# Kernel tuning notes

Measured on AMD Instinct MI355X. Metric: run time of the kernel, lower is better.

## Reference

```python
import jax, jax.numpy as jnp
import numpy as np

B, T, C, H = 2, 2048, 1024, 16
HS = C // H  # 64
EPS = 1e-5


def layernorm(x, g, b):
    mu = jnp.mean(x, axis=-1, keepdims=True)
    var = jnp.var(x, axis=-1, keepdims=True)
    return (x - mu) * jax.lax.rsqrt(var + EPS) * g + b


def setup_inputs() -> dict:
    key = jax.random.key(0)
    ks = jax.random.split(key, 12)
    s = lambda fan_in: 1.0 / np.sqrt(fan_in)
    inp = {
        'x':  jax.random.normal(ks[0], (B, T, C), dtype=jnp.float32),
        'Wq': jax.random.uniform(ks[1], (H, C, HS), jnp.float32, -s(C), s(C)),
        'Wk': jax.random.uniform(ks[2], (H, C, HS), jnp.float32, -s(C), s(C)),
        'Wv': jax.random.uniform(ks[3], (H, C, HS), jnp.float32, -s(C), s(C)),
        'Wp': jax.random.uniform(ks[4], (C, C), jnp.float32, -s(C), s(C)),
        'bp': jax.random.uniform(ks[5], (C,), jnp.float32, -s(C), s(C)),
        'W1': jax.random.uniform(ks[6], (C, 4 * C), jnp.float32, -s(C), s(C)),
        'b1': jax.random.uniform(ks[7], (4 * C,), jnp.float32, -s(C), s(C)),
        'W2': jax.random.uniform(ks[8], (4 * C, C), jnp.float32, -s(4 * C), s(4 * C)),
        'b2': jax.random.uniform(ks[9], (C,), jnp.float32, -s(4 * C), s(4 * C)),
        'g1': jnp.ones((C,), jnp.float32),
        'be1': jnp.zeros((C,), jnp.float32),
        'g2': jnp.ones((C,), jnp.float32),
        'be2': jnp.zeros((C,), jnp.float32),
    }
    return inp


def block(x, Wq, Wk, Wv, Wp, bp, W1, b1, W2, b2, g1, be1, g2, be2):
    # quirky residual structure: residual is taken from the post-LN tensor
    x = layernorm(x, g1, be1)
    # batched multi-head attention (all heads at once): [B,H,T,HS]
    q = jnp.einsum('btc,hcd->bhtd', x, Wq)
    k = jnp.einsum('btc,hcd->bhtd', x, Wk)
    v = jnp.einsum('btc,hcd->bhtd', x, Wv)
    # NOTE: original scales by full embedding dim C ** -0.5, not head_size
    scores = jnp.einsum('bhtd,bhsd->bhts', q, k) * (C ** -0.5)
    causal = jnp.tril(jnp.ones((T, T), dtype=bool))
    scores = jnp.where(causal, scores, -jnp.inf)
    wei = jax.nn.softmax(scores, axis=-1)  # dropout p=0 in eval
    out = jnp.einsum('bhts,bhsd->bhtd', wei, v)
    out = out.transpose(0, 2, 1, 3).reshape(B, T, C)  # concat heads
    out = out @ Wp + bp
    x = x + out
    x = layernorm(x, g2, be2)
    ff = jax.nn.relu(x @ W1 + b1) @ W2 + b2
    return x + ff


def reference(x, Wq, Wk, Wv, Wp, bp, W1, b1, W2, b2, g1, be1, g2, be2):
    return block(x, Wq, Wk, Wv, Wp, bp, W1, b1, W2, b2, g1, be1, g2, be2)
```

## Files before the change

kernel.cpp:

```cpp
#include <hip/hip_runtime.h>
#include <hip/hip_bf16.h>
#include <cstdint>
#include <cstddef>

typedef __attribute__((ext_vector_type(8))) short short8;
typedef __attribute__((ext_vector_type(4))) float f32x4;
typedef __attribute__((ext_vector_type(16))) float f32x16;
typedef unsigned int u32;
typedef unsigned short u16;

__device__ inline u16 f2b(float x) {
    union { float f; u32 u; } v; v.f = x;
    u32 u = v.u;
    u32 r = (u + 0x7fff + ((u >> 16) & 1)) >> 16;
    return (u16)r;
}
__device__ inline float b2f(u16 h) {
    union { u32 u; float f; } v; v.u = ((u32)h) << 16;
    return v.f;
}
__device__ inline u32 cvtpk(float lo, float hi) {
    u32 r; asm("v_cvt_pk_bf16_f32 %0, %1, %2" : "=v"(r) : "v"(lo), "v"(hi)); return r;
}
__device__ inline float ex2(float x) {
    float r; asm("v_exp_f32 %0, %1" : "=v"(r) : "v"(x)); return r;
}
__device__ inline void gll16(const void* g, void* l) {
    __builtin_amdgcn_global_load_lds(
        (const __attribute__((address_space(1))) void*)g,
        (__attribute__((address_space(3))) void*)l, 16, 0, 0);
}

__global__ __launch_bounds__(256) void repack_qkv_tiled(
    const float* __restrict__ Wq, const float* __restrict__ Wk, const float* __restrict__ Wv,
    u16* __restrict__ out)
{
    __shared__ u16 lds[64 * 72];
    const int tid = threadIdx.x;
    const int c0 = blockIdx.x * 64;
    const int sh = blockIdx.y;
    const int sel = sh >> 4, h = sh & 15;
    const float* W = (sel == 0) ? Wq : (sel == 1) ? Wk : Wv;
    #pragma unroll
    for (int it = 0; it < 4; ++it) {
        int idx = tid + it * 256;
        int c = idx >> 4, d4 = idx & 15;
        float4 v = *reinterpret_cast<const float4*>(&W[((size_t)(h * 1024 + c0 + c)) * 64 + d4 * 4]);
        lds[(d4 * 4 + 0) * 72 + c] = f2b(v.x);
        lds[(d4 * 4 + 1) * 72 + c] = f2b(v.y);
        lds[(d4 * 4 + 2) * 72 + c] = f2b(v.z);
        lds[(d4 * 4 + 3) * 72 + c] = f2b(v.w);
    }
    __syncthreads();
    #pragma unroll
    for (int it = 0; it < 2; ++it) {
        int idx = tid + it * 256;
        int d = idx >> 3, c8 = idx & 7;
        short8 s = *reinterpret_cast<const short8*>(&lds[d * 72 + c8 * 8]);
        *reinterpret_cast<short8*>(&out[((size_t)(sel * 1024 + h * 64 + d)) * 1024 + c0 + c8 * 8]) = s;
    }
}

__global__ __launch_bounds__(256) void trans_tiled(
    const float* __restrict__ in, u16* __restrict__ out, int P, int Q)
{
    __shared__ u16 lds[64 * 72];
    const int tid = threadIdx.x;
    const int p0 = blockIdx.x * 64, q0 = blockIdx.y * 64;
    #pragma unroll
    for (int it = 0; it < 4; ++it) {
        int idx = tid + it * 256;
        int p = idx >> 4, q4 = idx & 15;
        float4 v = *reinterpret_cast<const float4*>(&in[(size_t)(p0 + p) * Q + q0 + q4 * 4]);
        lds[(q4 * 4 + 0) * 72 + p] = f2b(v.x);
        lds[(q4 * 4 + 1) * 72 + p] = f2b(v.y);
        lds[(q4 * 4 + 2) * 72 + p] = f2b(v.z);
        lds[(q4 * 4 + 3) * 72 + p] = f2b(v.w);
    }
    __syncthreads();
    #pragma unroll
    for (int it = 0; it < 2; ++it) {
        int idx = tid + it * 256;
        int q = idx >> 3, p8 = idx & 7;
        short8 s = *reinterpret_cast<const short8*>(&lds[q * 72 + p8 * 8]);
        *reinterpret_cast<short8*>(&out[(size_t)(q0 + q) * P + p0 + p8 * 8]) = s;
    }
}

__global__ __launch_bounds__(256) void vt_kernel(
    const u16* __restrict__ qkv, u16* __restrict__ vt)
{
    __shared__ u16 lds[64 * 72];
    const int tid = threadIdx.x;
    const int s0 = blockIdx.x * 64, h = blockIdx.y, b = blockIdx.z;
    #pragma unroll
    for (int it = 0; it < 2; ++it) {
        int idx = tid + it * 256;
        int s = idx >> 3, d8 = idx & 7;
        short8 kv = *reinterpret_cast<const short8*>(
            &qkv[((size_t)(b * 2048 + s0 + s)) * 3072 + 2048 + h * 64 + d8 * 8]);
        #pragma unroll
        for (int j = 0; j < 8; ++j) lds[(d8 * 8 + j) * 72 + s] = (u16)kv[j];
    }
    __syncthreads();
    #pragma unroll
    for (int it = 0; it < 2; ++it) {
        int idx = tid + it * 256;
        int d = idx >> 3, s8 = idx & 7;
        short8 s = *reinterpret_cast<const short8*>(&lds[d * 72 + s8 * 8]);
        *reinterpret_cast<short8*>(&vt[((size_t)(b * 16 + h) * 64 + d) * 2048 + s0 + s8 * 8]) = s;
    }
}

__global__ __launch_bounds__(256) void ln_kernel(
    const float* __restrict__ x, const float* __restrict__ g, const float* __restrict__ be,
    float* __restrict__ yf, u16* __restrict__ yb)
{
    int row = blockIdx.x;
    const float4 v = reinterpret_cast<const float4*>(x + (size_t)row * 1024)[threadIdx.x];
    float s  = v.x + v.y + v.z + v.w;
    float s2 = v.x * v.x + v.y * v.y + v.z * v.z + v.w * v.w;
    #pragma unroll
    for (int o = 32; o >= 1; o >>= 1) { s += __shfl_xor(s, o); s2 += __shfl_xor(s2, o); }
    __shared__ float red[8];
    int w = threadIdx.x >> 6;
    if ((threadIdx.x & 63) == 0) { red[w] = s; red[4 + w] = s2; }
    __syncthreads();
    s  = red[0] + red[1] + red[2] + red[3];
    s2 = red[4] + red[5] + red[6] + red[7];
    float mu = s * (1.0f / 1024.0f);
    float var = s2 * (1.0f / 1024.0f) - mu * mu;
    float rs = rsqrtf(var + 1e-5f);
    const float4 gg = reinterpret_cast<const float4*>(g)[threadIdx.x];
    const float4 bb = reinterpret_cast<const float4*>(be)[threadIdx.x];
    float4 o;
    o.x = (v.x - mu) * rs * gg.x + bb.x;
    o.y = (v.y - mu) * rs * gg.y + bb.y;
    o.z = (v.z - mu) * rs * gg.z + bb.z;
    o.w = (v.w - mu) * rs * gg.w + bb.w;
    reinterpret_cast<float4*>(yf + (size_t)row * 1024)[threadIdx.x] = o;
    uint2 pk;
    pk.x = (u32)f2b(o.x) | ((u32)f2b(o.y) << 16);
    pk.y = (u32)f2b(o.z) | ((u32)f2b(o.w) << 16);
    reinterpret_cast<uint2*>(yb + (size_t)row * 1024)[threadIdx.x] = pk;
}

template<bool BIAS, bool RELU, bool RESID, bool OUTB>
__global__ __launch_bounds__(256) void gemm_bt(
    const u16* __restrict__ A, int lda,
    const u16* __restrict__ BT, int ldb,
    void* __restrict__ out, int ldo,
    const float* __restrict__ bias,
    const float* __restrict__ resid,
    int K)
{
    __shared__ __align__(16) char smem[64 * 1024];
    const int tid = threadIdx.x;
    const int lane = tid & 63, w = tid >> 6;
    const int wr = w >> 1, wc = w & 1;
    const int l15 = lane & 15, lq = lane >> 4;

    const int nx = gridDim.x;
    const int nwg = nx * gridDim.y;
    int orig = blockIdx.y * nx + blockIdx.x;
    int wgid = orig;
    if ((nwg & 7) == 0) wgid = (orig & 7) * (nwg >> 3) + (orig >> 3);
    const int m0 = (wgid / nx) * 128, n0 = (wgid % nx) * 128;

    auto stage = [&](int kt, int buf) {
        char* As = smem + buf * 32768;
        char* Bs = smem + buf * 32768 + 16384;
        #pragma unroll
        for (int it = 0; it < 4; ++it) {
            int slot = it * 256 + tid;
            int row = slot >> 3, c8 = (slot & 7) ^ (row & 7);
            gll16(A + (size_t)(m0 + row) * lda + kt + c8 * 8, As + (it * 256 + w * 64) * 16);
        }
        #pragma unroll
        for (int it = 0; it < 4; ++it) {
            int slot = it * 256 + tid;
            int row = slot >> 3, c8 = (slot & 7) ^ (row & 7);
            gll16(BT + (size_t)(n0 + row) * ldb + kt + c8 * 8, Bs + (it * 256 + w * 64) * 16);
        }
    };

    f32x4 acc[4][4] = {};
    const int nk = K >> 6;

    stage(0, 0);
    asm volatile("s_waitcnt vmcnt(0)" ::: "memory");
    __builtin_amdgcn_s_barrier();

    for (int t = 0; t < nk; ++t) {
        const char* As = smem + (t & 1) * 32768;
        const char* Bs = smem + (t & 1) * 32768 + 16384;
        if (t + 1 < nk) {
            stage((t + 1) << 6, (t + 1) & 1);
            asm volatile("s_waitcnt vmcnt(8)" ::: "memory");
        } else {
            asm volatile("s_waitcnt vmcnt(0)" ::: "memory");
        }
        __builtin_amdgcn_s_barrier();

        #pragma unroll
        for (int kk = 0; kk < 2; ++kk) {
            const int sc = kk * 4 + lq;
            short8 a[4], b[4];
            #pragma unroll
            for (int mi = 0; mi < 4; ++mi) {
                int row = wr * 64 + mi * 16 + l15;
                a[mi] = *reinterpret_cast<const short8*>(As + row * 128 + ((sc ^ (row & 7)) << 4));
            }
            #pragma unroll
            for (int ni = 0; ni < 4; ++ni) {
                int row = wc * 64 + ni * 16 + l15;
                b[ni] = *reinterpret_cast<const short8*>(Bs + row * 128 + ((sc ^ (row & 7)) << 4));
            }
            #pragma unroll
            for (int mi = 0; mi < 4; ++mi)
                #pragma unroll
                for (int ni = 0; ni < 4; ++ni)
                    acc[mi][ni] = __builtin_amdgcn_mfma_f32_16x16x32_bf16(a[mi], b[ni], acc[mi][ni], 0, 0, 0);
        }

        asm volatile("" ::: "memory");
        __builtin_amdgcn_s_barrier();
    }

    #pragma unroll
    for (int mi = 0; mi < 4; ++mi) {
        #pragma unroll
        for (int ni = 0; ni < 4; ++ni) {
            int col = n0 + wc * 64 + ni * 16 + l15;
            float bv = BIAS ? bias[col] : 0.0f;
            #pragma unroll
            for (int r = 0; r < 4; ++r) {
                int row = m0 + wr * 64 + mi * 16 + lq * 4 + r;
                float v = acc[mi][ni][r] + bv;
                if (RELU) v = v > 0.0f ? v : 0.0f;
                if (RESID) v += resid[(size_t)row * ldo + col];
                if (OUTB) ((u16*)out)[(size_t)row * ldo + col] = f2b(v);
                else      ((float*)out)[(size_t)row * ldo + col] = v;
            }
        }
    }
}

template<bool BIAS, bool RELU, bool OUTB>
__global__ __launch_bounds__(512) void gemm_bt256(
    const u16* __restrict__ A, int lda,
    const u16* __restrict__ BT, int ldb,
    void* __restrict__ out, int ldo,
    const float* __restrict__ bias,
    int K)
{
    __shared__ __align__(16) char smem[128 * 1024];
    const int tid = threadIdx.x;
    const int lane = tid & 63, wid = tid >> 6;
    const int wm = wid >> 2, wn = wid & 3;
    const int l15 = lane & 15, lq = lane >> 4;

    const int nx = gridDim.x;
    const int nwg = nx * gridDim.y;
    int orig = blockIdx.y * nx + blockIdx.x;
    int wgid = orig;
    if ((nwg & 7) == 0) wgid = (orig & 7) * (nwg >> 3) + (orig >> 3);
    const int m0 = (wgid / nx) * 256, n0 = (wgid % nx) * 256;

    auto stage = [&](int kt, int buf) {
        char* As = smem + buf * 65536;
        char* Bs = smem + buf * 65536 + 32768;
        #pragma unroll
        for (int i = 0; i < 4; ++i) {
            int slot = i * 512 + tid;
            int row = slot >> 3, c8 = (slot & 7) ^ (row & 7);
            gll16(A + (size_t)(m0 + row) * lda + kt + c8 * 8, As + (i * 512 + wid * 64) * 16);
        }
        #pragma unroll
        for (int i = 0; i < 4; ++i) {
            int slot = i * 512 + tid;
            int row = slot >> 3, c8 = (slot & 7) ^ (row & 7);
            gll16(BT + (size_t)(n0 + row) * ldb + kt + c8 * 8, Bs + (i * 512 + wid * 64) * 16);
        }
    };

    f32x4 acc[8][4] = {};
    const int nk = K >> 6;

    stage(0, 0);
    asm volatile("s_waitcnt vmcnt(0)" ::: "memory");
    __builtin_amdgcn_s_barrier();

    for (int t = 0; t < nk; ++t) {
        const char* As = smem + (t & 1) * 65536;
        const char* Bs = smem + (t & 1) * 65536 + 32768;
        if (t + 1 < nk) {
            stage((t + 1) << 6, (t + 1) & 1);
            asm volatile("s_waitcnt vmcnt(8)" ::: "memory");
        } else {
            asm volatile("s_waitcnt vmcnt(0)" ::: "memory");
        }
        __builtin_amdgcn_s_barrier();

        #pragma unroll
        for (int kk = 0; kk < 2; ++kk) {
            const int sc = kk * 4 + lq;
            short8 a[8], b[4];
            #pragma unroll
            for (int mi = 0; mi < 8; ++mi) {
                int row = wm * 128 + mi * 16 + l15;
                a[mi] = *reinterpret_cast<const short8*>(As + row * 128 + ((sc ^ (row & 7)) << 4));
            }
            #pragma unroll
            for (int ni = 0; ni < 4; ++ni) {
                int row = wn * 64 + ni * 16 + l15;
                b[ni] = *reinterpret_cast<const short8*>(Bs + row * 128 + ((sc ^ (row & 7)) << 4));
            }
            #pragma unroll
            for (int mi = 0; mi < 8; ++mi)
                #pragma unroll
                for (int ni = 0; ni < 4; ++ni)
                    acc[mi][ni] = __builtin_amdgcn_mfma_f32_16x16x32_bf16(a[mi], b[ni], acc[mi][ni], 0, 0, 0);
        }

        asm volatile("" ::: "memory");
        __builtin_amdgcn_s_barrier();
    }

    #pragma unroll
    for (int mi = 0; mi < 8; ++mi) {
        #pragma unroll
        for (int ni = 0; ni < 4; ++ni) {
            int col = n0 + wn * 64 + ni * 16 + l15;
            float bv = BIAS ? bias[col] : 0.0f;
            #pragma unroll
            for (int r = 0; r < 4; ++r) {
                int row = m0 + wm * 128 + mi * 16 + lq * 4 + r;
                float v = acc[mi][ni][r] + bv;
                if (RELU) v = v > 0.0f ? v : 0.0f;
                if (OUTB) ((u16*)out)[(size_t)row * ldo + col] = f2b(v);
                else      ((float*)out)[(size_t)row * ldo + col] = v;
            }
        }
    }
}

__global__ __launch_bounds__(256, 2) void attn_kernel(
    const u16* __restrict__ qkv, const u16* __restrict__ vt, u16* __restrict__ att)
{
    __shared__ __align__(16) char smem[48 * 1024];
    char* Kb0 = smem;
    char* Kb1 = smem + 8192;
    char* Vb0 = smem + 16384;
    char* Vb1 = smem + 24576;
    char* Ost = smem + 32768;

    const int tid = threadIdx.x, lane = tid & 63, w = tid >> 6;
    const int l31 = lane & 31, hi = lane >> 5;
    const int bh = blockIdx.x;
    const int b = bh >> 4, h = bh & 15;
    const size_t base = (size_t)b * 2048;
    const int kcol = 1024 + h * 64;
    const u16* vtp = vt + (size_t)bh * 64 * 2048;
    const float SC = 0.03125f * 1.44269504f;

    auto stage = [&](int st, char* kb, char* vb) {
        #pragma unroll
        for (int i = 0; i < 2; ++i) {
            int seg = w * 2 + i;
            int slot = seg * 64 + lane;
            int s = slot >> 3, d8p = slot & 7;
            gll16(qkv + (base + st * 64 + s) * 3072 + kcol + ((d8p ^ (s & 7)) * 8),
                  kb + seg * 1024);
            int d = s, s8p = d8p;
            gll16(vtp + (size_t)d * 2048 + st * 64 + ((s8p ^ (d & 7)) * 8),
                  vb + seg * 1024);
        }
    };

    for (int pass = 0; pass < 2; ++pass) {
        const int qbi = pass ? (int)blockIdx.y : 15 - (int)blockIdx.y;
        const int q0w = qbi * 128 + w * 32;
        const int nst = 2 * qbi + 2;
        const int qg = q0w + l31;

        short8 qf[4];
        {
            const u16* qp = qkv + (base + q0w + l31) * 3072 + h * 64 + hi * 8;
            #pragma unroll
            for (int dc = 0; dc < 4; ++dc) {
                short8 q = *reinterpret_cast<const short8*>(qp + dc * 16);
                #pragma unroll
                for (int j = 0; j < 8; j += 2) {
                    u32 pk = cvtpk(b2f((u16)q[j]) * SC, b2f((u16)q[j + 1]) * SC);
                    q[j]     = (short)(pk & 0xffff);
                    q[j + 1] = (short)(pk >> 16);
                }
                qf[dc] = q;
            }
        }

        f32x16 oT[2] = {};
        float m = -1e30f, lsum = 0.0f;

        stage(0, Kb0, Vb0);
        __syncthreads();

        for (int st = 0; st < nst; ++st) {
            char* kb = (st & 1) ? Kb1 : Kb0;
            char* vb = (st & 1) ? Vb1 : Vb0;
            if (st + 1 < nst) stage(st + 1, (st & 1) ? Kb0 : Kb1, (st & 1) ? Vb0 : Vb1);

            f32x16 sa[2] = {};
            #pragma unroll
            for (int dc = 0; dc < 4; ++dc) {
                #pragma unroll
                for (int sb = 0; sb < 2; ++sb) {
                    int s = sb * 32 + l31;
                    int slot = (dc * 2 + hi) ^ (s & 7);
                    short8 kf = *reinterpret_cast<const short8*>(kb + s * 128 + slot * 16);
                    sa[sb] = __builtin_amdgcn_mfma_f32_32x32x16_bf16(kf, qf[dc], sa[sb], 0, 0, 0);
                }
            }

            if (st >= nst - 2) {
                #pragma unroll
                for (int sb = 0; sb < 2; ++sb)
                    #pragma unroll
                    for (int r = 0; r < 16; ++r) {
                        int sg = st * 64 + sb * 32 + (r & 3) + 8 * (r >> 2) + 4 * hi;
                        if (sg > qg) sa[sb][r] = -1e30f;
                    }
            }

            float t8[8];
            #pragma unroll
            for (int i = 0; i < 8; ++i)
                t8[i] = fmaxf(fmaxf(sa[0][i], sa[0][i + 8]), fmaxf(sa[1][i], sa[1][i + 8]));
            float t4a = fmaxf(t8[0], t8[4]), t4b = fmaxf(t8[1], t8[5]);
            float t4c = fmaxf(t8[2], t8[6]), t4d = fmaxf(t8[3], t8[7]);
            float mx = fmaxf(fmaxf(t4a, t4b), fmaxf(t4c, t4d));
            mx = fmaxf(mx, __shfl_xor(mx, 32));

            if (!__all(mx <= m + 8.0f)) {
                float nm = fmaxf(m, mx);
                float sf = ex2(m - nm);
                m = nm;
                lsum *= sf;
                #pragma unroll
                for (int dt = 0; dt < 2; ++dt)
                    #pragma unroll
                    for (int r = 0; r < 16; ++r) oT[dt][r] *= sf;
            }

            #pragma unroll
            for (int sb = 0; sb < 2; ++sb)
                #pragma unroll
                for (int r = 0; r < 16; ++r) sa[sb][r] = ex2(sa[sb][r] - m);
            float s8_[8];
            #pragma unroll
            for (int i = 0; i < 8; ++i)
                s8_[i] = (sa[0][i] + sa[0][i + 8]) + (sa[1][i] + sa[1][i + 8]);
            float s4a = s8_[0] + s8_[4], s4b = s8_[1] + s8_[5];
            float s4c = s8_[2] + s8_[6], s4d = s8_[3] + s8_[7];
            float ps = (s4a + s4b) + (s4c + s4d);
            ps += __shfl_xor(ps, 32);
            lsum += ps;

            u32 pkE[4][2], pkO[4][2];
            #pragma unroll
            for (int sc = 0; sc < 4; ++sc) {
                const int sb = sc >> 1, rb = 8 * (sc & 1);
                #pragma unroll
                for (int c = 0; c < 2; ++c) {
                    pkE[sc][c] = cvtpk(sa[sb][rb + 2 * c], sa[sb][rb + 2 * c + 1]);
                    pkO[sc][c] = cvtpk(sa[sb][rb + 4 + 2 * c], sa[sb][rb + 4 + 2 * c + 1]);
                }
            }

            #pragma unroll
            for (int sc = 0; sc < 4; ++sc) {
                u32 wd[4];
                #pragma unroll
                for (int ww = 0; ww < 4; ++ww) {
                    const int c = ww & 1;
                    u32 own  = hi ? pkO[sc][c] : pkE[sc][c];
                    u32 send = hi ? pkE[sc][c] : pkO[sc][c];
                    u32 ex = (u32)__shfl_xor((int)send, 32);
                    wd[ww] = ((ww >> 1) == hi) ? own : ex;
                }
                union { u32 u[4]; short8 s8; } pb_;
                pb_.u[0] = wd[0]; pb_.u[1] = wd[1]; pb_.u[2] = wd[2]; pb_.u[3] = wd[3];
                #pragma unroll
                for (int dt = 0; dt < 2; ++dt) {
                    int d = dt * 32 + l31;
                    int slot = (sc * 2 + hi) ^ (d & 7);
                    short8 vf = *reinterpret_cast<const short8*>(vb + d * 128 + slot * 16);
                    oT[dt] = __builtin_amdgcn_mfma_f32_32x32x16_bf16(vf, pb_.s8, oT[dt], 0, 0, 0);
                }
            }
            __syncthreads();
        }

        {
            float inv = 1.0f / lsum;
            char* ob = Ost + w * 4096;
            #pragma unroll
            for (int dt = 0; dt < 2; ++dt)
                #pragma unroll
                for (int rp = 0; rp < 8; ++rp) {
                    int r = rp * 2;
                    int d = dt * 32 + (r & 3) + 8 * (r >> 2) + 4 * hi;
                    u32 pk2 = cvtpk(oT[dt][r] * inv, oT[dt][r + 1] * inv);
                    int byte = l31 * 128 + ((((d >> 3) ^ (l31 & 7)) << 4)) + (d & 7) * 2;
                    *reinterpret_cast<u32*>(ob + byte) = pk2;
                }
            int q = lane >> 1, half = lane & 1;
            size_t grow = (base + q0w - w * 32 + (w * 32 + q)) * 1024 + h * 64 + half * 32;
            #pragma unroll
            for (int c = 0; c < 4; ++c) {
                int chunk = half * 4 + c;
                int byte = q * 128 + ((chunk ^ (q & 7)) << 4);
                float4 vv = *reinterpret_cast<const float4*>(ob + byte);
                *reinterpret_cast<float4*>(att + grow + c * 8) = vv;
            }
        }
    }
}

extern "C" void kernel_launch(void* const* d_in, const int* in_sizes, int n_in,
                              void* d_out, int out_size, void* d_ws, size_t ws_size,
                              hipStream_t stream)
{
    const float* x   = (const float*)d_in[0];
    const float* Wq  = (const float*)d_in[1];
    const float* Wk  = (const float*)d_in[2];
    const float* Wv  = (const float*)d_in[3];
    const float* Wp  = (const float*)d_in[4];
    const float* bp  = (const float*)d_in[5];
    const float* W1  = (const float*)d_in[6];
    const float* b1  = (const float*)d_in[7];
    const float* W2  = (const float*)d_in[8];
    const float* b2  = (const float*)d_in[9];
    const float* g1  = (const float*)d_in[10];
    const float* be1 = (const float*)d_in[11];
    const float* g2  = (const float*)d_in[12];
    const float* be2 = (const float*)d_in[13];
    float* out = (float*)d_out;

    char* ws = (char*)d_ws;
    u16*   wqkvT = (u16*)(ws + 0);
    u16*   wpT   = (u16*)(ws + 6291456);
    u16*   w1T   = (u16*)(ws + 8388608);
    u16*   w2T   = (u16*)(ws + 16777216);
    float* xlnF  = (float*)(ws + 25165824);
    u16*   xlnB  = (u16*)(ws + 41943040);
    u16*   qkv   = (u16*)(ws + 50331648);
    float* x2    = (float*)(ws + 50331648);
    u16*   hbuf  = (u16*)(ws + 50331648);
    u16*   attb  = (u16*)(ws + 75497472);
    float* yF    = (float*)(ws + 83886080);
    u16*   vtb   = (u16*)(ws + 83886080);
    u16*   yB    = xlnB;

    repack_qkv_tiled<<<dim3(16, 48), 256, 0, stream>>>(Wq, Wk, Wv, wqkvT);
    trans_tiled<<<dim3(16, 16), 256, 0, stream>>>(Wp, wpT, 1024, 1024);
    trans_tiled<<<dim3(16, 64), 256, 0, stream>>>(W1, w1T, 1024, 4096);
    trans_tiled<<<dim3(64, 16), 256, 0, stream>>>(W2, w2T, 4096, 1024);

    ln_kernel<<<4096, 256, 0, stream>>>(x, g1, be1, xlnF, xlnB);

    gemm_bt256<false, false, true><<<dim3(12, 16), 512, 0, stream>>>(
        xlnB, 1024, wqkvT, 1024, qkv, 3072, nullptr, 1024);

    vt_kernel<<<dim3(32, 16, 2), 256, 0, stream>>>(qkv, vtb);
    attn_kernel<<<dim3(32, 8), 256, 0, stream>>>(qkv, vtb, attb);

    gemm_bt<true, false, true, false><<<dim3(8, 32), 256, 0, stream>>>(
        attb, 1024, wpT, 1024, x2, 1024, bp, xlnF, 1024);

    ln_kernel<<<4096, 256, 0, stream>>>(x2, g2, be2, yF, yB);

    gemm_bt256<true, true, true><<<dim3(16, 16), 512, 0, stream>>>(
        yB, 1024, w1T, 1024, hbuf, 4096, b1, 1024);

    gemm_bt<true, false, true, false><<<dim3(8, 32), 256, 0, stream>>>(
        hbuf, 4096, w2T, 4096, out, 1024, b2, yF, 4096);
}
```

Measured before the change: 221.9 us.

## Split FF2 GEMM along K into two slices and unroll attention passes into grid

```diff
diff --git a/kernel.cpp b/kernel.cpp
--- a/kernel.cpp
+++ b/kernel.cpp
@@ -246,6 +246,121 @@
     }
 }
 
+__global__ __launch_bounds__(256) void gemm_ff2(
+    const u16* __restrict__ A,
+    const u16* __restrict__ BT,
+    float* __restrict__ outp,
+    float* __restrict__ p1,
+    const float* __restrict__ bias,
+    const float* __restrict__ resid)
+{
+    __shared__ __align__(16) char smem[64 * 1024];
+    const int tid = threadIdx.x;
+    const int lane = tid & 63, w = tid >> 6;
+    const int wr = w >> 1, wc = w & 1;
+    const int l15 = lane & 15, lq = lane >> 4;
+    const int z = blockIdx.z;
+    const int koff = z * 2048;
+
+    const int nx = gridDim.x;
+    const int nwg = nx * gridDim.y;
+    int orig = blockIdx.y * nx + blockIdx.x;
+    int wgid = (orig & 7) * (nwg >> 3) + (orig >> 3);
+    const int m0 = (wgid / nx) * 128, n0 = (wgid % nx) * 128;
+
+    auto stage = [&](int kt, int buf) {
+        char* As = smem + buf * 32768;
+        char* Bs = smem + buf * 32768 + 16384;
+        #pragma unroll
+        for (int it = 0; it < 4; ++it) {
+            int slot = it * 256 + tid;
+            int row = slot >> 3, c8 = (slot & 7) ^ (row & 7);
+            gll16(A + (size_t)(m0 + row) * 4096 + koff + kt + c8 * 8, As + (it * 256 + w * 64) * 16);
+        }
+        #pragma unroll
+        for (int it = 0; it < 4; ++it) {
+            int slot = it * 256 + tid;
+            int row = slot >> 3, c8 = (slot & 7) ^ (row & 7);
+            gll16(BT + (size_t)(n0 + row) * 4096 + koff + kt + c8 * 8, Bs + (it * 256 + w * 64) * 16);
+        }
+    };
+
+    f32x4 acc[4][4] = {};
+    const int nk = 32;
+
+    stage(0, 0);
+    asm volatile("s_waitcnt vmcnt(0)" ::: "memory");
+    __builtin_amdgcn_s_barrier();
+
+    for (int t = 0; t < nk; ++t) {
+        const char* As = smem + (t & 1) * 32768;
+        const char* Bs = smem + (t & 1) * 32768 + 16384;
+        if (t + 1 < nk) {
+            stage((t + 1) << 6, (t + 1) & 1);
+            asm volatile("s_waitcnt vmcnt(8)" ::: "memory");
+        } else {
+            asm volatile("s_waitcnt vmcnt(0)" ::: "memory");
+        }
+        __builtin_amdgcn_s_barrier();
+
+        #pragma unroll
+        for (int kk = 0; kk < 2; ++kk) {
+            const int sc = kk * 4 + lq;
+            short8 a[4], b[4];
+            #pragma unroll
+            for (int mi = 0; mi < 4; ++mi) {
+                int row = wr * 64 + mi * 16 + l15;
+                a[mi] = *reinterpret_cast<const short8*>(As + row * 128 + ((sc ^ (row & 7)) << 4));
+            }
+            #pragma unroll
+            for (int ni = 0; ni < 4; ++ni) {
+                int row = wc * 64 + ni * 16 + l15;
+                b[ni] = *reinterpret_cast<const short8*>(Bs + row * 128 + ((sc ^ (row & 7)) << 4));
+            }
+            #pragma unroll
+            for (int mi = 0; mi < 4; ++mi)
+                #pragma unroll
+                for (int ni = 0; ni < 4; ++ni)
+                    acc[mi][ni] = __builtin_amdgcn_mfma_f32_16x16x32_bf16(a[mi], b[ni], acc[mi][ni], 0, 0, 0);
+        }
+
+        asm volatile("" ::: "memory");
+        __builtin_amdgcn_s_barrier();
+    }
+
+    #pragma unroll
+    for (int mi = 0; mi < 4; ++mi) {
+        #pragma unroll
+        for (int ni = 0; ni < 4; ++ni) {
+            int col = n0 + wc * 64 + ni * 16 + l15;
+            #pragma unroll
+            for (int r = 0; r < 4; ++r) {
+                int row = m0 + wr * 64 + mi * 16 + lq * 4 + r;
+                float v = acc[mi][ni][r];
+                if (z == 0) {
+                    v += bias[col] + resid[(size_t)row * 1024 + col];
+                    outp[(size_t)row * 1024 + col] = v;
+                } else {
+                    p1[(size_t)row * 1024 + col] = v;
+                }
+            }
+        }
+    }
+}
+
+__global__ __launch_bounds__(256) void add_kernel(
+    float* __restrict__ out, const float* __restrict__ p1, int n4)
+{
+    int i = blockIdx.x * 256 + threadIdx.x;
+    int stride = gridDim.x * 256;
+    for (; i < n4; i += stride) {
+        float4 a = reinterpret_cast<float4*>(out)[i];
+        float4 b = reinterpret_cast<const float4*>(p1)[i];
+        a.x += b.x; a.y += b.y; a.z += b.z; a.w += b.w;
+        reinterpret_cast<float4*>(out)[i] = a;
+    }
+}
+
 template<bool BIAS, bool RELU, bool OUTB>
 __global__ __launch_bounds__(512) void gemm_bt256(
     const u16* __restrict__ A, int lda,
@@ -358,11 +473,17 @@
     const int tid = threadIdx.x, lane = tid & 63, w = tid >> 6;
     const int l31 = lane & 31, hi = lane >> 5;
     const int bh = blockIdx.x;
+    const int by = blockIdx.y;
+    const int qbi = (by < 8) ? (15 - by) : (by - 8);
     const int b = bh >> 4, h = bh & 15;
     const size_t base = (size_t)b * 2048;
     const int kcol = 1024 + h * 64;
     const u16* vtp = vt + (size_t)bh * 64 * 2048;
     const float SC = 0.03125f * 1.44269504f;
+
+    const int q0w = qbi * 128 + w * 32;
+    const int nst = 2 * qbi + 2;
+    const int qg = q0w + l31;
 
     auto stage = [&](int st, char* kb, char* vb) {
         #pragma unroll
@@ -378,152 +499,145 @@
         }
     };
 
-    for (int pass = 0; pass < 2; ++pass) {
-        const int qbi = pass ? (int)blockIdx.y : 15 - (int)blockIdx.y;
-        const int q0w = qbi * 128 + w * 32;
-        const int nst = 2 * qbi + 2;
-        const int qg = q0w + l31;
-
-        short8 qf[4];
-        {
-            const u16* qp = qkv + (base + q0w + l31) * 3072 + h * 64 + hi * 8;
-            #pragma unroll
-            for (int dc = 0; dc < 4; ++dc) {
-                short8 q = *reinterpret_cast<const short8*>(qp + dc * 16);
-                #pragma unroll
-                for (int j = 0; j < 8; j += 2) {
-                    u32 pk = cvtpk(b2f((u16)q[j]) * SC, b2f((u16)q[j + 1]) * SC);
-                    q[j]     = (short)(pk & 0xffff);
-                    q[j + 1] = (short)(pk >> 16);
-                }
-                qf[dc] = q;
-            }
-        }
-
-        f32x16 oT[2] = {};
-        float m = -1e30f, lsum = 0.0f;
-
-        stage(0, Kb0, Vb0);
-        __syncthreads();
-
-        for (int st = 0; st < nst; ++st) {
-            char* kb = (st & 1) ? Kb1 : Kb0;
-            char* vb = (st & 1) ? Vb1 : Vb0;
-            if (st + 1 < nst) stage(st + 1, (st & 1) ? Kb0 : Kb1, (st & 1) ? Vb0 : Vb1);
-
-            f32x16 sa[2] = {};
-            #pragma unroll
-            for (int dc = 0; dc < 4; ++dc) {
-                #pragma unroll
-                for (int sb = 0; sb < 2; ++sb) {
-                    int s = sb * 32 + l31;
-                    int slot = (dc * 2 + hi) ^ (s & 7);
-                    short8 kf = *reinterpret_cast<const short8*>(kb + s * 128 + slot * 16);
-                    sa[sb] = __builtin_amdgcn_mfma_f32_32x32x16_bf16(kf, qf[dc], sa[sb], 0, 0, 0);
-                }
-            }
-
-            if (st >= nst - 2) {
-                #pragma unroll
-                for (int sb = 0; sb < 2; ++sb)
-                    #pragma unroll
-                    for (int r = 0; r < 16; ++r) {
-                        int sg = st * 64 + sb * 32 + (r & 3) + 8 * (r >> 2) + 4 * hi;
-                        if (sg > qg) sa[sb][r] = -1e30f;
-                    }
-            }
-
-            float t8[8];
-            #pragma unroll
-            for (int i = 0; i < 8; ++i)
-                t8[i] = fmaxf(fmaxf(sa[0][i], sa[0][i + 8]), fmaxf(sa[1][i], sa[1][i + 8]));
-            float t4a = fmaxf(t8[0], t8[4]), t4b = fmaxf(t8[1], t8[5]);
-            float t4c = fmaxf(t8[2], t8[6]), t4d = fmaxf(t8[3], t8[7]);
-            float mx = fmaxf(fmaxf(t4a, t4b), fmaxf(t4c, t4d));
-            mx = fmaxf(mx, __shfl_xor(mx, 32));
-
-            if (!__all(mx <= m + 8.0f)) {
-                float nm = fmaxf(m, mx);
-                float sf = ex2(m - nm);
-                m = nm;
-                lsum *= sf;
-                #pragma unroll
-                for (int dt = 0; dt < 2; ++dt)
-                    #pragma unroll
-                    for (int r = 0; r < 16; ++r) oT[dt][r] *= sf;
-            }
-
+    short8 qf[4];
+    {
+        const u16* qp = qkv + (base + q0w + l31) * 3072 + h * 64 + hi * 8;
+        #pragma unroll
+        for (int dc = 0; dc < 4; ++dc) {
+            short8 q = *reinterpret_cast<const short8*>(qp + dc * 16);
+            #pragma unroll
+            for (int j = 0; j < 8; j += 2) {
+                u32 pk = cvtpk(b2f((u16)q[j]) * SC, b2f((u16)q[j + 1]) * SC);
+                q[j]     = (short)(pk & 0xffff);
+                q[j + 1] = (short)(pk >> 16);
+            }
+            qf[dc] = q;
+        }
+    }
+
+    f32x16 oT[2] = {};
+    float m = -1e30f, lsum = 0.0f;
+
+    stage(0, Kb0, Vb0);
+    __syncthreads();
+
+    for (int st = 0; st < nst; ++st) {
+        char* kb = (st & 1) ? Kb1 : Kb0;
+        char* vb = (st & 1) ? Vb1 : Vb0;
+        if (st + 1 < nst) stage(st + 1, (st & 1) ? Kb0 : Kb1, (st & 1) ? Vb0 : Vb1);
+
+        f32x16 sa[2] = {};
+        #pragma unroll
+        for (int dc = 0; dc < 4; ++dc) {
+            #pragma unroll
+            for (int sb = 0; sb < 2; ++sb) {
+                int s = sb * 32 + l31;
+                int slot = (dc * 2 + hi) ^ (s & 7);
+                short8 kf = *reinterpret_cast<const short8*>(kb + s * 128 + slot * 16);
+                sa[sb] = __builtin_amdgcn_mfma_f32_32x32x16_bf16(kf, qf[dc], sa[sb], 0, 0, 0);
+            }
+        }
+
+        if (st >= nst - 2) {
             #pragma unroll
             for (int sb = 0; sb < 2; ++sb)
                 #pragma unroll
-                for (int r = 0; r < 16; ++r) sa[sb][r] = ex2(sa[sb][r] - m);
-            float s8_[8];
-            #pragma unroll
-            for (int i = 0; i < 8; ++i)
-                s8_[i] = (sa[0][i] + sa[0][i + 8]) + (sa[1][i] + sa[1][i + 8]);
-            float s4a = s8_[0] + s8_[4], s4b = s8_[1] + s8_[5];
-            float s4c = s8_[2] + s8_[6], s4d = s8_[3] + s8_[7];
-            float ps = (s4a + s4b) + (s4c + s4d);
-            ps += __shfl_xor(ps, 32);
-            lsum += ps;
-
-            u32 pkE[4][2], pkO[4][2];
-            #pragma unroll
-            for (int sc = 0; sc < 4; ++sc) {
-                const int sb = sc >> 1, rb = 8 * (sc & 1);
-                #pragma unroll
-                for (int c = 0; c < 2; ++c) {
-                    pkE[sc][c] = cvtpk(sa[sb][rb + 2 * c], sa[sb][rb + 2 * c + 1]);
-                    pkO[sc][c] = cvtpk(sa[sb][rb + 4 + 2 * c], sa[sb][rb + 4 + 2 * c + 1]);
+                for (int r = 0; r < 16; ++r) {
+                    int sg = st * 64 + sb * 32 + (r & 3) + 8 * (r >> 2) + 4 * hi;
+                    if (sg > qg) sa[sb][r] = -1e30f;
                 }
-            }
-
-            #pragma unroll
-            for (int sc = 0; sc < 4; ++sc) {
-                u32 wd[4];
-                #pragma unroll
-                for (int ww = 0; ww < 4; ++ww) {
-                    const int c = ww & 1;
-                    u32 own  = hi ? pkO[sc][c] : pkE[sc][c];
-                    u32 send = hi ? pkE[sc][c] : pkO[sc][c];
-                    u32 ex = (u32)__shfl_xor((int)send, 32);
-                    wd[ww] = ((ww >> 1) == hi) ? own : ex;
-                }
-                union { u32 u[4]; short8 s8; } pb_;
-                pb_.u[0] = wd[0]; pb_.u[1] = wd[1]; pb_.u[2] = wd[2]; pb_.u[3] = wd[3];
-                #pragma unroll
-                for (int dt = 0; dt < 2; ++dt) {
-                    int d = dt * 32 + l31;
-                    int slot = (sc * 2 + hi) ^ (d & 7);
-                    short8 vf = *reinterpret_cast<const short8*>(vb + d * 128 + slot * 16);
-                    oT[dt] = __builtin_amdgcn_mfma_f32_32x32x16_bf16(vf, pb_.s8, oT[dt], 0, 0, 0);
-                }
-            }
-            __syncthreads();
-        }
-
-        {
-            float inv = 1.0f / lsum;
-            char* ob = Ost + w * 4096;
+        }
+
+        float t8[8];
+        #pragma unroll
+        for (int i = 0; i < 8; ++i)
+            t8[i] = fmaxf(fmaxf(sa[0][i], sa[0][i + 8]), fmaxf(sa[1][i], sa[1][i + 8]));
+        float t4a = fmaxf(t8[0], t8[4]), t4b = fmaxf(t8[1], t8[5]);
+        float t4c = fmaxf(t8[2], t8[6]), t4d = fmaxf(t8[3], t8[7]);
+        float mx = fmaxf(fmaxf(t4a, t4b), fmaxf(t4c, t4d));
+        mx = fmaxf(mx, __shfl_xor(mx, 32));
+
+        if (!__all(mx <= m + 8.0f)) {
+            float nm = fmaxf(m, mx);
+            float sf = ex2(m - nm);
+            m = nm;
+            lsum *= sf;
             #pragma unroll
             for (int dt = 0; dt < 2; ++dt)
                 #pragma unroll
-                for (int rp = 0; rp < 8; ++rp) {
-                    int r = rp * 2;
-                    int d = dt * 32 + (r & 3) + 8 * (r >> 2) + 4 * hi;
-                    u32 pk2 = cvtpk(oT[dt][r] * inv, oT[dt][r + 1] * inv);
-                    int byte = l31 * 128 + ((((d >> 3) ^ (l31 & 7)) << 4)) + (d & 7) * 2;
-                    *reinterpret_cast<u32*>(ob + byte) = pk2;
-                }
-            int q = lane >> 1, half = lane & 1;
-            size_t grow = (base + q0w - w * 32 + (w * 32 + q)) * 1024 + h * 64 + half * 32;
-            #pragma unroll
-            for (int c = 0; c < 4; ++c) {
-                int chunk = half * 4 + c;
-                int byte = q * 128 + ((chunk ^ (q & 7)) << 4);
-                float4 vv = *reinterpret_cast<const float4*>(ob + byte);
-                *reinterpret_cast<float4*>(att + grow + c * 8) = vv;
-            }
+                for (int r = 0; r < 16; ++r) oT[dt][r] *= sf;
+        }
+
+        #pragma unroll
+        for (int sb = 0; sb < 2; ++sb)
+            #pragma unroll
+            for (int r = 0; r < 16; ++r) sa[sb][r] = ex2(sa[sb][r] - m);
+        float s8_[8];
+        #pragma unroll
+        for (int i = 0; i < 8; ++i)
+            s8_[i] = (sa[0][i] + sa[0][i + 8]) + (sa[1][i] + sa[1][i + 8]);
+        float s4a = s8_[0] + s8_[4], s4b = s8_[1] + s8_[5];
+        float s4c = s8_[2] + s8_[6], s4d = s8_[3] + s8_[7];
+        float ps = (s4a + s4b) + (s4c + s4d);
+        ps += __shfl_xor(ps, 32);
+        lsum += ps;
+
+        u32 pkE[4][2], pkO[4][2];
+        #pragma unroll
+        for (int sc = 0; sc < 4; ++sc) {
+            const int sb = sc >> 1, rb = 8 * (sc & 1);
+            #pragma unroll
+            for (int c = 0; c < 2; ++c) {
+                pkE[sc][c] = cvtpk(sa[sb][rb + 2 * c], sa[sb][rb + 2 * c + 1]);
+                pkO[sc][c] = cvtpk(sa[sb][rb + 4 + 2 * c], sa[sb][rb + 4 + 2 * c + 1]);
+            }
+        }
+
+        #pragma unroll
+        for (int sc = 0; sc < 4; ++sc) {
+            u32 wd[4];
+            #pragma unroll
+            for (int ww = 0; ww < 4; ++ww) {
+                const int c = ww & 1;
+                u32 own  = hi ? pkO[sc][c] : pkE[sc][c];
+                u32 send = hi ? pkE[sc][c] : pkO[sc][c];
+                u32 ex = (u32)__shfl_xor((int)send, 32);
+                wd[ww] = ((ww >> 1) == hi) ? own : ex;
+            }
+            union { u32 u[4]; short8 s8; } pb_;
+            pb_.u[0] = wd[0]; pb_.u[1] = wd[1]; pb_.u[2] = wd[2]; pb_.u[3] = wd[3];
+            #pragma unroll
+            for (int dt = 0; dt < 2; ++dt) {
+                int d = dt * 32 + l31;
+                int slot = (sc * 2 + hi) ^ (d & 7);
+                short8 vf = *reinterpret_cast<const short8*>(vb + d * 128 + slot * 16);
+                oT[dt] = __builtin_amdgcn_mfma_f32_32x32x16_bf16(vf, pb_.s8, oT[dt], 0, 0, 0);
+            }
+        }
+        __syncthreads();
+    }
+
+    {
+        float inv = 1.0f / lsum;
+        char* ob = Ost + w * 4096;
+        #pragma unroll
+        for (int dt = 0; dt < 2; ++dt)
+            #pragma unroll
+            for (int rp = 0; rp < 8; ++rp) {
+                int r = rp * 2;
+                int d = dt * 32 + (r & 3) + 8 * (r >> 2) + 4 * hi;
+                u32 pk2 = cvtpk(oT[dt][r] * inv, oT[dt][r + 1] * inv);
+                int byte = l31 * 128 + ((((d >> 3) ^ (l31 & 7)) << 4)) + (d & 7) * 2;
+                *reinterpret_cast<u32*>(ob + byte) = pk2;
+            }
+        int q = lane >> 1, half = lane & 1;
+        size_t grow = (base + q0w + q) * 1024 + h * 64 + half * 32;
+        #pragma unroll
+        for (int c = 0; c < 4; ++c) {
+            int chunk = half * 4 + c;
+            int byte = q * 128 + ((chunk ^ (q & 7)) << 4);
+            float4 vv = *reinterpret_cast<const float4*>(ob + byte);
+            *reinterpret_cast<float4*>(att + grow + c * 8) = vv;
         }
     }
 }
@@ -554,6 +668,7 @@
     u16*   w1T   = (u16*)(ws + 8388608);
     u16*   w2T   = (u16*)(ws + 16777216);
     float* xlnF  = (float*)(ws + 25165824);
+    float* p1f   = (float*)(ws + 25165824);
     u16*   xlnB  = (u16*)(ws + 41943040);
     u16*   qkv   = (u16*)(ws + 50331648);
     float* x2    = (float*)(ws + 50331648);
@@ -574,7 +689,7 @@
         xlnB, 1024, wqkvT, 1024, qkv, 3072, nullptr, 1024);
 
     vt_kernel<<<dim3(32, 16, 2), 256, 0, stream>>>(qkv, vtb);
-    attn_kernel<<<dim3(32, 8), 256, 0, stream>>>(qkv, vtb, attb);
+    attn_kernel<<<dim3(32, 16), 256, 0, stream>>>(qkv, vtb, attb);
 
     gemm_bt<true, false, true, false><<<dim3(8, 32), 256, 0, stream>>>(
         attb, 1024, wpT, 1024, x2, 1024, bp, xlnF, 1024);
@@ -584,6 +699,6 @@
     gemm_bt256<true, true, true><<<dim3(16, 16), 512, 0, stream>>>(
         yB, 1024, w1T, 1024, hbuf, 4096, b1, 1024);
 
-    gemm_bt<true, false, true, false><<<dim3(8, 32), 256, 0, stream>>>(
-        hbuf, 4096, w2T, 4096, out, 1024, b2, yF, 4096);
-}
+    gemm_ff2<<<dim3(8, 32, 2), 256, 0, stream>>>(hbuf, w2T, out, p1f, b2, yF);
+    add_kernel<<<2048, 256, 0, stream>>>(out, p1f, 1048576);
+}
```

New measurement: 238.2 us. +7.4%, slower.

## Run both causal query blocks concurrently in one 512-thread attention block

Applied to the files above, without the earlier changes.

```diff
diff --git a/kernel.cpp b/kernel.cpp
--- a/kernel.cpp
+++ b/kernel.cpp
@@ -345,10 +345,10 @@
     }
 }
 
-__global__ __launch_bounds__(256, 2) void attn_kernel(
+__global__ __launch_bounds__(512, 1) void attn_kernel(
     const u16* __restrict__ qkv, const u16* __restrict__ vt, u16* __restrict__ att)
 {
-    __shared__ __align__(16) char smem[48 * 1024];
+    __shared__ __align__(16) char smem[64 * 1024];
     char* Kb0 = smem;
     char* Kb1 = smem + 8192;
     char* Vb0 = smem + 16384;
@@ -358,59 +358,57 @@
     const int tid = threadIdx.x, lane = tid & 63, w = tid >> 6;
     const int l31 = lane & 31, hi = lane >> 5;
     const int bh = blockIdx.x;
+    const int by = blockIdx.y;
     const int b = bh >> 4, h = bh & 15;
     const size_t base = (size_t)b * 2048;
     const int kcol = 1024 + h * 64;
     const u16* vtp = vt + (size_t)bh * 64 * 2048;
     const float SC = 0.03125f * 1.44269504f;
 
+    const int qbi = (w < 4) ? (15 - by) : by;
+    const int wq = w & 3;
+    const int q0w = qbi * 128 + wq * 32;
+    const int nst_w = 2 * qbi + 2;
+    const int nst_max = 2 * (15 - by) + 2;
+    const int qg = q0w + l31;
+
     auto stage = [&](int st, char* kb, char* vb) {
-        #pragma unroll
-        for (int i = 0; i < 2; ++i) {
-            int seg = w * 2 + i;
-            int slot = seg * 64 + lane;
-            int s = slot >> 3, d8p = slot & 7;
-            gll16(qkv + (base + st * 64 + s) * 3072 + kcol + ((d8p ^ (s & 7)) * 8),
-                  kb + seg * 1024);
-            int d = s, s8p = d8p;
-            gll16(vtp + (size_t)d * 2048 + st * 64 + ((s8p ^ (d & 7)) * 8),
-                  vb + seg * 1024);
-        }
+        int slot = w * 64 + lane;
+        int s = slot >> 3, d8p = slot & 7;
+        gll16(qkv + (base + st * 64 + s) * 3072 + kcol + ((d8p ^ (s & 7)) * 8),
+              kb + w * 1024);
+        gll16(vtp + (size_t)s * 2048 + st * 64 + ((d8p ^ (s & 7)) * 8),
+              vb + w * 1024);
     };
 
-    for (int pass = 0; pass < 2; ++pass) {
-        const int qbi = pass ? (int)blockIdx.y : 15 - (int)blockIdx.y;
-        const int q0w = qbi * 128 + w * 32;
-        const int nst = 2 * qbi + 2;
-        const int qg = q0w + l31;
-
-        short8 qf[4];
-        {
-            const u16* qp = qkv + (base + q0w + l31) * 3072 + h * 64 + hi * 8;
-            #pragma unroll
-            for (int dc = 0; dc < 4; ++dc) {
-                short8 q = *reinterpret_cast<const short8*>(qp + dc * 16);
-                #pragma unroll
-                for (int j = 0; j < 8; j += 2) {
-                    u32 pk = cvtpk(b2f((u16)q[j]) * SC, b2f((u16)q[j + 1]) * SC);
-                    q[j]     = (short)(pk & 0xffff);
-                    q[j + 1] = (short)(pk >> 16);
-                }
-                qf[dc] = q;
-            }
-        }
-
-        f32x16 oT[2] = {};
-        float m = -1e30f, lsum = 0.0f;
-
-        stage(0, Kb0, Vb0);
-        __syncthreads();
-
-        for (int st = 0; st < nst; ++st) {
-            char* kb = (st & 1) ? Kb1 : Kb0;
-            char* vb = (st & 1) ? Vb1 : Vb0;
-            if (st + 1 < nst) stage(st + 1, (st & 1) ? Kb0 : Kb1, (st & 1) ? Vb0 : Vb1);
-
+    short8 qf[4];
+    {
+        const u16* qp = qkv + (base + q0w + l31) * 3072 + h * 64 + hi * 8;
+        #pragma unroll
+        for (int dc = 0; dc < 4; ++dc) {
+            short8 q = *reinterpret_cast<const short8*>(qp + dc * 16);
+            #pragma unroll
+            for (int j = 0; j < 8; j += 2) {
+                u32 pk = cvtpk(b2f((u16)q[j]) * SC, b2f((u16)q[j + 1]) * SC);
+                q[j]     = (short)(pk & 0xffff);
+                q[j + 1] = (short)(pk >> 16);
+            }
+            qf[dc] = q;
+        }
+    }
+
+    f32x16 oT[2] = {};
+    float m = -1e30f, lsum = 0.0f;
+
+    stage(0, Kb0, Vb0);
+    __syncthreads();
+
+    for (int st = 0; st < nst_max; ++st) {
+        char* kb = (st & 1) ? Kb1 : Kb0;
+        char* vb = (st & 1) ? Vb1 : Vb0;
+        if (st + 1 < nst_max) stage(st + 1, (st & 1) ? Kb0 : Kb1, (st & 1) ? Vb0 : Vb1);
+
+        if (st < nst_w) {
             f32x16 sa[2] = {};
             #pragma unroll
             for (int dc = 0; dc < 4; ++dc) {
@@ -423,7 +421,7 @@
                 }
             }
 
-            if (st >= nst - 2) {
+            if (st >= nst_w - 2) {
                 #pragma unroll
                 for (int sb = 0; sb < 2; ++sb)
                     #pragma unroll
@@ -499,31 +497,31 @@
                     oT[dt] = __builtin_amdgcn_mfma_f32_32x32x16_bf16(vf, pb_.s8, oT[dt], 0, 0, 0);
                 }
             }
-            __syncthreads();
-        }
-
-        {
-            float inv = 1.0f / lsum;
-            char* ob = Ost + w * 4096;
-            #pragma unroll
-            for (int dt = 0; dt < 2; ++dt)
-                #pragma unroll
-                for (int rp = 0; rp < 8; ++rp) {
-                    int r = rp * 2;
-                    int d = dt * 32 + (r & 3) + 8 * (r >> 2) + 4 * hi;
-                    u32 pk2 = cvtpk(oT[dt][r] * inv, oT[dt][r + 1] * inv);
-                    int byte = l31 * 128 + ((((d >> 3) ^ (l31 & 7)) << 4)) + (d & 7) * 2;
-                    *reinterpret_cast<u32*>(ob + byte) = pk2;
-                }
-            int q = lane >> 1, half = lane & 1;
-            size_t grow = (base + q0w - w * 32 + (w * 32 + q)) * 1024 + h * 64 + half * 32;
-            #pragma unroll
-            for (int c = 0; c < 4; ++c) {
-                int chunk = half * 4 + c;
-                int byte = q * 128 + ((chunk ^ (q & 7)) << 4);
-                float4 vv = *reinterpret_cast<const float4*>(ob + byte);
-                *reinterpret_cast<float4*>(att + grow + c * 8) = vv;
-            }
+        }
+        __syncthreads();
+    }
+
+    {
+        float inv = 1.0f / lsum;
+        char* ob = Ost + w * 4096;
+        #pragma unroll
+        for (int dt = 0; dt < 2; ++dt)
+            #pragma unroll
+            for (int rp = 0; rp < 8; ++rp) {
+                int r = rp * 2;
+                int d = dt * 32 + (r & 3) + 8 * (r >> 2) + 4 * hi;
+                u32 pk2 = cvtpk(oT[dt][r] * inv, oT[dt][r + 1] * inv);
+                int byte = l31 * 128 + ((((d >> 3) ^ (l31 & 7)) << 4)) + (d & 7) * 2;
+                *reinterpret_cast<u32*>(ob + byte) = pk2;
+            }
+        int q = lane >> 1, half = lane & 1;
+        size_t grow = (base + q0w + q) * 1024 + h * 64 + half * 32;
+        #pragma unroll
+        for (int c = 0; c < 4; ++c) {
+            int chunk = half * 4 + c;
+            int byte = q * 128 + ((chunk ^ (q & 7)) << 4);
+            float4 vv = *reinterpret_cast<const float4*>(ob + byte);
+            *reinterpret_cast<float4*>(att + grow + c * 8) = vv;
         }
     }
 }
@@ -574,7 +572,7 @@
         xlnB, 1024, wqkvT, 1024, qkv, 3072, nullptr, 1024);
 
     vt_kernel<<<dim3(32, 16, 2), 256, 0, stream>>>(qkv, vtb);
-    attn_kernel<<<dim3(32, 8), 256, 0, stream>>>(qkv, vtb, attb);
+    attn_kernel<<<dim3(32, 8), 512, 0, stream>>>(qkv, vtb, attb);
 
     gemm_bt<true, false, true, false><<<dim3(8, 32), 256, 0, stream>>>(
         attb, 1024, wpT, 1024, x2, 1024, bp, xlnF, 1024);
```

After: 223.5 us. About the same (+0.7%).
